# Kernel tuning notes

Hardware: AMD Instinct MI355X
Metric: run time of the kernel (lower is better)

## Reference

```python
import jax, jax.numpy as jnp
import numpy as np

FREQ = 10000.0

def _abs_pos(T, d, freq):
    # AP[t, 2i] = sin(t / freq**(2i/d)), AP[t, 2i+1] = cos(...), i in [0, T//2)
    pos = jnp.arange(T, dtype=jnp.float32)[:, None]          # [T,1]
    i = jnp.arange(T // 2, dtype=jnp.float32)[None, :]       # [1,T/2]
    angle = pos / (freq ** (2.0 * i / d))                    # [T,T/2]
    return jnp.stack([jnp.sin(angle), jnp.cos(angle)], axis=-1).reshape(T, T)

def setup_inputs() -> dict:
    key = jax.random.key(0)
    k0, k1, k2, k3, k4 = jax.random.split(key, 5)
    T, d, H, dh = 4096, 1024, 8, 128
    s = 1.0 / np.sqrt(d).astype(np.float32)
    return {
        "x": jax.random.normal(k0, (T, d), jnp.float32),
        "Wq": jax.random.normal(k1, (H, dh, d), jnp.float32) * s,
        "Wk": jax.random.normal(k2, (H, dh, d), jnp.float32) * s,
        "Wv": jax.random.normal(k3, (H, dh, d), jnp.float32) * s,
        "Wout": jax.random.normal(k4, (d, H * dh), jnp.float32) * s,
    }

def reference(x, Wq, Wk, Wv, Wout):
    # x: [T,d]; Wq/Wk/Wv: [H,dh,d] (torch Linear weight layout, bias=False); Wout: [d, H*dh]
    T, d = x.shape
    Q = jnp.einsum('td,hed->hte', x, Wq)                     # [H,T,dh]
    K = jnp.einsum('td,hed->hte', x, Wk)
    V = jnp.einsum('td,hed->hte', x, Wv)
    energies = jnp.einsum('hte,hse->hts', Q, K)              # [H,T,T] (no 1/sqrt(dh) scaling, as in source)
    energies = energies + _abs_pos(T, d, FREQ)[None]         # absolute sinusoidal bias added to scores
    att = jax.nn.softmax(energies, axis=-1)                  # [H,T,T]
    # dropout(p=0.5) is identity in eval mode; reference runs in eval mode
    y = jnp.einsum('hts,hse->hte', att, V)                   # [H,T,dh]
    y = jnp.transpose(y, (1, 0, 2)).reshape(T, -1)           # concat heads along feature dim -> [T, H*dh]
    y = y @ Wout.T                                           # [T,d]
    return y, att[-1]                                        # source returns last head's att_weights
```

## Files before the change

kernel.cpp:

```cpp
#include <hip/hip_runtime.h>
#include <math.h>

#define Tn 4096
#define Dm 1024
#define Hn 8
#define DH 128

typedef __bf16 bf16x8 __attribute__((ext_vector_type(8)));
typedef float f32x4 __attribute__((ext_vector_type(4)));

#define LOG2E 1.4426950408889634f
#define WEXP 0.025952563241307518f
#define WDECAY 0.31622776601683794f
#define PIO2 1.5707963267948966f

#define MFMA(a, b, c) __builtin_amdgcn_mfma_f32_16x16x32_bf16((a), (b), (c), 0, 0, 0)

#define GLOAD_LDS(g, l) __builtin_amdgcn_global_load_lds( \
    (__attribute__((address_space(1))) void*)(void*)(g),  \
    (__attribute__((address_space(3))) void*)(l), 16, 0, 0)

__global__ __launch_bounds__(256)
void split_kernel(const float* __restrict__ in, __bf16* __restrict__ hi,
                  __bf16* __restrict__ lo, int n4) {
    int idx = blockIdx.x * 256 + threadIdx.x;
    if (idx >= n4) return;
    float4 v = ((const float4*)in)[idx];
    __attribute__((aligned(8))) __bf16 h[4], l[4];
    h[0] = (__bf16)v.x; h[1] = (__bf16)v.y; h[2] = (__bf16)v.z; h[3] = (__bf16)v.w;
    l[0] = (__bf16)(v.x - (float)h[0]);
    l[1] = (__bf16)(v.y - (float)h[1]);
    l[2] = (__bf16)(v.z - (float)h[2]);
    l[3] = (__bf16)(v.w - (float)h[3]);
    *(float2*)&hi[(size_t)idx * 4] = *(float2*)h;
    *(float2*)&lo[(size_t)idx * 4] = *(float2*)l;
}

__global__ __launch_bounds__(256)
void vtrans_kernel(const __bf16* __restrict__ V, __bf16* __restrict__ Vt) {
    __shared__ __bf16 tile[64][80];
    int h = blockIdx.z, t0 = blockIdx.x * 64, e0 = blockIdx.y * 64;
    const __bf16* Vh = V + (size_t)h * Tn * DH;
    __bf16* Vth = Vt + (size_t)h * DH * Tn;
#pragma unroll
    for (int p = 0; p < 2; ++p) {
        int r = (threadIdx.x >> 3) + p * 32;
        int c = (threadIdx.x & 7) * 8;
        *(float4*)&tile[r][c] = *(const float4*)&Vh[(size_t)(t0 + r) * DH + e0 + c];
    }
    __syncthreads();
#pragma unroll
    for (int p = 0; p < 2; ++p) {
        int r = (threadIdx.x >> 3) + p * 32;
        int c = (threadIdx.x & 7) * 8;
        __attribute__((aligned(16))) __bf16 tmp[8];
#pragma unroll
        for (int j = 0; j < 8; ++j) tmp[j] = tile[c + j][r];
        *(float4*)&Vth[(size_t)(e0 + r) * Tn + t0 + c] = *(float4*)tmp;
    }
}

__device__ __forceinline__
void gemm_body(__bf16 (*smem)[128 * 32],
               const __bf16* __restrict__ Ahi, const __bf16* __restrict__ Alo,
               const __bf16* __restrict__ Bhi, const __bf16* __restrict__ Blo,
               int ldA, int ldB, int K, int m0, int n0, f32x4 acc[4][4]) {
    int tid = threadIdx.x;
    int lane = tid & 63, wid = tid >> 6;
    int wm = (wid >> 1) * 64, wn = (wid & 1) * 64;
    int lm = lane & 15, q = lane >> 4;
    int lr = lane >> 2;
    int lc = (lane & 3) * 8;
    const bool split = (Alo != nullptr);
    for (int k0 = 0; k0 < K; k0 += 32) {
        __syncthreads();
#pragma unroll
        for (int p = 0; p < 128; p += 64) {
            int rb = p + wid * 16;
            int r = rb + lr;
            GLOAD_LDS(&Ahi[(size_t)(m0 + r) * ldA + k0 + lc], &smem[0][rb * 32]);
            GLOAD_LDS(&Bhi[(size_t)(n0 + r) * ldB + k0 + lc], &smem[2][rb * 32]);
            if (split) {
                GLOAD_LDS(&Alo[(size_t)(m0 + r) * ldA + k0 + lc], &smem[1][rb * 32]);
                GLOAD_LDS(&Blo[(size_t)(n0 + r) * ldB + k0 + lc], &smem[3][rb * 32]);
            }
        }
        __syncthreads();
        bf16x8 ah[4], bh[4], al[4], bl[4];
#pragma unroll
        for (int mt = 0; mt < 4; ++mt) {
            ah[mt] = *(const bf16x8*)&smem[0][(wm + mt * 16 + lm) * 32 + q * 8];
            if (split)
                al[mt] = *(const bf16x8*)&smem[1][(wm + mt * 16 + lm) * 32 + q * 8];
        }
#pragma unroll
        for (int nt = 0; nt < 4; ++nt) {
            bh[nt] = *(const bf16x8*)&smem[2][(wn + nt * 16 + lm) * 32 + q * 8];
            if (split)
                bl[nt] = *(const bf16x8*)&smem[3][(wn + nt * 16 + lm) * 32 + q * 8];
        }
#pragma unroll
        for (int mt = 0; mt < 4; ++mt)
#pragma unroll
            for (int nt = 0; nt < 4; ++nt) {
                acc[mt][nt] = MFMA(ah[mt], bh[nt], acc[mt][nt]);
                if (split) {
                    acc[mt][nt] = MFMA(ah[mt], bl[nt], acc[mt][nt]);
                    acc[mt][nt] = MFMA(al[mt], bh[nt], acc[mt][nt]);
                }
            }
    }
}

__global__ __launch_bounds__(256)
void qkv_kernel(const __bf16* __restrict__ xhi, const __bf16* __restrict__ xlo,
                const __bf16* __restrict__ Wqh, const __bf16* __restrict__ Wql,
                const __bf16* __restrict__ Wkh, const __bf16* __restrict__ Wkl,
                const __bf16* __restrict__ Wvh, const __bf16* __restrict__ Wvl,
                __bf16* __restrict__ Qh, __bf16* __restrict__ Ql,
                __bf16* __restrict__ Kh, __bf16* __restrict__ Kl,
                __bf16* __restrict__ Vb) {
    __shared__ __align__(16) __bf16 smem[4][128 * 32];
    int z = blockIdx.z;
    const __bf16* Bh = (z == 0) ? Wqh : (z == 1) ? Wkh : Wvh;
    const __bf16* Bl = (z == 0) ? Wql : (z == 1) ? Wkl : Wvl;
    __bf16* Oh = (z == 0) ? Qh : (z == 1) ? Kh : Vb;
    __bf16* Ol = (z == 0) ? Ql : (z == 1) ? Kl : nullptr;
    int m0 = blockIdx.y * 128, n0 = blockIdx.x * 128;
    int tid = threadIdx.x, lane = tid & 63, wid = tid >> 6;
    int wm = (wid >> 1) * 64, wn = (wid & 1) * 64;
    int lm = lane & 15, q = lane >> 4;
    f32x4 acc[4][4];
#pragma unroll
    for (int i = 0; i < 4; ++i)
#pragma unroll
        for (int j = 0; j < 4; ++j) acc[i][j] = (f32x4){0.f, 0.f, 0.f, 0.f};
    gemm_body(smem, xhi, xlo, Bh, Bl, Dm, Dm, Dm, m0, n0, acc);
#pragma unroll
    for (int mt = 0; mt < 4; ++mt)
#pragma unroll
        for (int r = 0; r < 4; ++r) {
            int grow = m0 + wm + mt * 16 + q * 4 + r;
#pragma unroll
            for (int nt = 0; nt < 4; ++nt) {
                int gc = n0 + wn + nt * 16 + lm;
                int h = gc >> 7, e = gc & 127;
                size_t o = ((size_t)h * Tn + grow) * DH + e;
                float v = acc[mt][nt][r];
                __bf16 hv = (__bf16)v;
                Oh[o] = hv;
                if (Ol) Ol[o] = (__bf16)(v - (float)hv);
            }
        }
}

__global__ __launch_bounds__(256)
void gemm_out(const __bf16* __restrict__ Ahi, const __bf16* __restrict__ Alo,
              const __bf16* __restrict__ Bhi, const __bf16* __restrict__ Blo,
              float* __restrict__ C) {
    __shared__ __align__(16) __bf16 smem[4][128 * 32];
    int m0 = blockIdx.y * 128, n0 = blockIdx.x * 128;
    int tid = threadIdx.x, lane = tid & 63, wid = tid >> 6;
    int wm = (wid >> 1) * 64, wn = (wid & 1) * 64;
    int lm = lane & 15, q = lane >> 4;
    f32x4 acc[4][4];
#pragma unroll
    for (int i = 0; i < 4; ++i)
#pragma unroll
        for (int j = 0; j < 4; ++j) acc[i][j] = (f32x4){0.f, 0.f, 0.f, 0.f};
    gemm_body(smem, Ahi, Alo, Bhi, Blo, Dm, Dm, Dm, m0, n0, acc);
#pragma unroll
    for (int mt = 0; mt < 4; ++mt)
#pragma unroll
        for (int r = 0; r < 4; ++r) {
            int grow = m0 + wm + mt * 16 + q * 4 + r;
#pragma unroll
            for (int nt = 0; nt < 4; ++nt)
                C[(size_t)grow * Dm + n0 + wn + nt * 16 + lm] = acc[mt][nt][r];
        }
}

#define QK_STEP(SET, BUF, QIDX, NIT, NKC)                                     \
    {                                                                          \
        *(float4*)&Ks[BUF][0][sr][scc]      = SET##h0;                         \
        *(float4*)&Ks[BUF][1][sr][scc]      = SET##l0;                         \
        *(float4*)&Ks[BUF][0][sr + 64][scc] = SET##h1;                         \
        *(float4*)&Ks[BUF][1][sr + 64][scc] = SET##l1;                         \
        __syncthreads();                                                       \
        {                                                                      \
            size_t go0 = (size_t)((NIT) * 128 + sr) * DH + (NKC) * 32 + scc;   \
            size_t go1 = go0 + (size_t)64 * DH;                                \
            SET##h0 = *(const float4*)&Kh[go0];                                \
            SET##l0 = *(const float4*)&Kl[go0];                                \
            SET##h1 = *(const float4*)&Kh[go1];                                \
            SET##l1 = *(const float4*)&Kl[go1];                                \
        }                                                                      \
        __builtin_amdgcn_s_setprio(1);                                         \
        _Pragma("unroll")                                                      \
        for (int nt = 0; nt < 8; ++nt) {                                       \
            bf16x8 kbh = *(const bf16x8*)&Ks[BUF][0][nt * 16 + lm][q * 8];     \
            bf16x8 kbl = *(const bf16x8*)&Ks[BUF][1][nt * 16 + lm][q * 8];     \
            accS[nt] = MFMA(qfh[QIDX], kbh, accS[nt]);                         \
            accS[nt] = MFMA(qfh[QIDX], kbl, accS[nt]);                         \
            accS[nt] = MFMA(qfl[QIDX], kbh, accS[nt]);                         \
        }                                                                      \
        __builtin_amdgcn_s_setprio(0);                                         \
    }

__global__ __launch_bounds__(256, 2)
void flash_kernel(const __bf16* __restrict__ Qhi, const __bf16* __restrict__ Qlo,
                  const __bf16* __restrict__ Khi, const __bf16* __restrict__ Klo,
                  const __bf16* __restrict__ Vt, float* __restrict__ Opart,
                  float* __restrict__ mPart, float* __restrict__ lPart) {
    __shared__ __bf16 Ks[2][2][128][40];
    __shared__ __bf16 Ps[64][132];
    int bid = blockIdx.x;
    int h = bid & 7;
    int g = (bid >> 3) & 1;
    int m0 = (bid >> 4) * 64;
    int it0 = g * 16;
    const size_t TD = (size_t)Tn * DH;
    const __bf16* Qh = Qhi + h * TD;
    const __bf16* Ql = Qlo + h * TD;
    const __bf16* Kh = Khi + h * TD;
    const __bf16* Kl = Klo + h * TD;
    const __bf16* Vh = Vt + h * TD;
    float* Og = Opart + (size_t)g * Tn * Dm;

    int tid = threadIdx.x;
    int lane = tid & 63, wid = tid >> 6;
    int lm = lane & 15, q = lane >> 4;
    int wr0 = wid * 16;

    bf16x8 qfh[4], qfl[4];
#pragma unroll
    for (int kc = 0; kc < 4; ++kc) {
        size_t o = (size_t)(m0 + wr0 + lm) * DH + kc * 32 + q * 8;
        qfh[kc] = *(const bf16x8*)&Qh[o];
        qfl[kc] = *(const bf16x8*)&Ql[o];
    }

    f32x4 accO[8];
#pragma unroll
    for (int nt = 0; nt < 8; ++nt) accO[nt] = (f32x4){0.f, 0.f, 0.f, 0.f};
    float mrow[4], lrow[4];
#pragma unroll
    for (int r = 0; r < 4; ++r) { mrow[r] = -3.0e38f; lrow[r] = 0.f; }

    int sr = tid >> 2;
    int scc = (tid & 3) * 8;
    bool iscos = (lm & 1);
    float wv[8];
#pragma unroll
    for (int nt = 0; nt < 8; ++nt)
        wv[nt] = exp2f(-(float)(((g << 11) + nt * 16 + lm) >> 1) * WEXP);
    float tf[4];
#pragma unroll
    for (int r = 0; r < 4; ++r) tf[r] = (float)(m0 + wr0 + q * 4 + r);

    size_t voff[8];
#pragma unroll
    for (int nt = 0; nt < 8; ++nt)
        voff[nt] = (size_t)(nt * 16 + lm) * Tn + q * 8;

    float4 kah0, kal0, kah1, kal1, kbh0, kbl0, kbh1, kbl1;
    {
        size_t g0 = (size_t)(it0 * 128 + sr) * DH + scc;
        size_t g1 = g0 + (size_t)64 * DH;
        kah0 = *(const float4*)&Kh[g0]; kal0 = *(const float4*)&Kl[g0];
        kah1 = *(const float4*)&Kh[g1]; kal1 = *(const float4*)&Kl[g1];
        size_t h0_ = g0 + 32, h1_ = g1 + 32;
        kbh0 = *(const float4*)&Kh[h0_]; kbl0 = *(const float4*)&Kl[h0_];
        kbh1 = *(const float4*)&Kh[h1_]; kbl1 = *(const float4*)&Kl[h1_];
    }

    for (int it = it0; it < it0 + 16; ++it) {
        int s0 = it * 128;
        int itn = (it < it0 + 15) ? it + 1 : it;
        f32x4 accS[8];
#pragma unroll
        for (int nt = 0; nt < 8; ++nt) accS[nt] = (f32x4){0.f, 0.f, 0.f, 0.f};

        QK_STEP(ka, 0, 0, it, 2)
        QK_STEP(kb, 1, 1, it, 3)
        QK_STEP(ka, 0, 2, itn, 0)
        QK_STEP(kb, 1, 3, itn, 1)

        bf16x8 vrel[8];
#pragma unroll
        for (int nt = 0; nt < 8; ++nt)
            vrel[nt] = *(const bf16x8*)&Vh[voff[nt] + s0];

        float rmax[4];
#pragma unroll
        for (int r = 0; r < 4; ++r) {
            float mx = -3.0e38f;
#pragma unroll
            for (int nt = 0; nt < 8; ++nt) {
                float ang = tf[r] * wv[nt];
                float b = __sinf(iscos ? ang + PIO2 : ang);
                float v = accS[nt][r] + b;
                accS[nt][r] = v;
                mx = fmaxf(mx, v);
            }
            rmax[r] = mx;
        }
#pragma unroll
        for (int off = 1; off < 16; off <<= 1)
#pragma unroll
            for (int r = 0; r < 4; ++r)
                rmax[r] = fmaxf(rmax[r], __shfl_xor(rmax[r], off));
        float alpha[4], rsum[4];
#pragma unroll
        for (int r = 0; r < 4; ++r) {
            float mn = fmaxf(mrow[r], rmax[r]);
            alpha[r] = exp2f((mrow[r] - mn) * LOG2E);
            mrow[r] = mn;
            rsum[r] = 0.f;
        }
#pragma unroll
        for (int nt = 0; nt < 8; ++nt)
#pragma unroll
            for (int r = 0; r < 4; ++r) {
                float p = exp2f((accS[nt][r] - mrow[r]) * LOG2E);
                accS[nt][r] = p;
                rsum[r] += p;
            }
#pragma unroll
        for (int off = 1; off < 16; off <<= 1)
#pragma unroll
            for (int r = 0; r < 4; ++r)
                rsum[r] += __shfl_xor(rsum[r], off);
#pragma unroll
        for (int r = 0; r < 4; ++r)
            lrow[r] = lrow[r] * alpha[r] + rsum[r];
#pragma unroll
        for (int nt = 0; nt < 8; ++nt)
#pragma unroll
            for (int r = 0; r < 4; ++r)
                accO[nt][r] *= alpha[r];

#pragma unroll
        for (int nt = 0; nt < 8; ++nt)
#pragma unroll
            for (int r = 0; r < 4; ++r)
                Ps[wr0 + q * 4 + r][nt * 16 + lm] = (__bf16)accS[nt][r];

#pragma unroll
        for (int kc = 0; kc < 4; ++kc) {
            bf16x8 pa = *(const bf16x8*)&Ps[wr0 + lm][kc * 32 + q * 8];
            bf16x8 vcur[8];
#pragma unroll
            for (int nt = 0; nt < 8; ++nt) vcur[nt] = vrel[nt];
            if (kc < 3) {
#pragma unroll
                for (int nt = 0; nt < 8; ++nt)
                    vrel[nt] = *(const bf16x8*)&Vh[voff[nt] + s0 + (kc + 1) * 32];
            }
            __builtin_amdgcn_s_setprio(1);
#pragma unroll
            for (int nt = 0; nt < 8; ++nt)
                accO[nt] = MFMA(pa, vcur[nt], accO[nt]);
            __builtin_amdgcn_s_setprio(0);
        }

#pragma unroll
        for (int nt = 0; nt < 8; ++nt) wv[nt] *= WDECAY;
    }

#pragma unroll
    for (int r = 0; r < 4; ++r) {
        int t = m0 + wr0 + q * 4 + r;
#pragma unroll
        for (int nt = 0; nt < 8; ++nt)
            Og[(size_t)t * Dm + h * DH + nt * 16 + lm] = accO[nt][r];
        if (lm == 0) {
            mPart[(size_t)(g * Hn + h) * Tn + t] = mrow[r];
            lPart[(size_t)(g * Hn + h) * Tn + t] = lrow[r];
        }
    }
}

__global__ __launch_bounds__(256)
void combine_kernel(const float* __restrict__ Opart,
                    const float* __restrict__ mPart, const float* __restrict__ lPart,
                    __bf16* __restrict__ yhi, __bf16* __restrict__ ylo,
                    float* __restrict__ mM, float* __restrict__ lL) {
    int idx = blockIdx.x * 256 + threadIdx.x;
    int t = idx >> 8;
    int c4 = idx & 255;
    int c = c4 * 4;
    int h = c >> 7;
    float m0 = mPart[(size_t)h * Tn + t];
    float m1 = mPart[(size_t)(Hn + h) * Tn + t];
    float l0 = lPart[(size_t)h * Tn + t];
    float l1 = lPart[(size_t)(Hn + h) * Tn + t];
    float m = fmaxf(m0, m1);
    float w0 = exp2f((m0 - m) * LOG2E);
    float w1 = exp2f((m1 - m) * LOG2E);
    float l = l0 * w0 + l1 * w1;
    float inv = 1.0f / l;
    w0 *= inv; w1 *= inv;
    float4 a = ((const float4*)Opart)[idx];
    float4 b = ((const float4*)(Opart + (size_t)Tn * Dm))[idx];
    float y[4] = {a.x * w0 + b.x * w1, a.y * w0 + b.y * w1,
                  a.z * w0 + b.z * w1, a.w * w0 + b.w * w1};
    __attribute__((aligned(8))) __bf16 hh[4], ll[4];
#pragma unroll
    for (int j = 0; j < 4; ++j) {
        hh[j] = (__bf16)y[j];
        ll[j] = (__bf16)(y[j] - (float)hh[j]);
    }
    *(float2*)&yhi[(size_t)idx * 4] = *(float2*)hh;
    *(float2*)&ylo[(size_t)idx * 4] = *(float2*)ll;
    if (h == 7 && (c & 127) == 0) { mM[t] = m; lL[t] = l; }
}

__global__ __launch_bounds__(256)
void att_kernel(const __bf16* __restrict__ Ahi, const __bf16* __restrict__ Alo,
                const __bf16* __restrict__ Bhi, const __bf16* __restrict__ Blo,
                const float* __restrict__ mM, const float* __restrict__ lL,
                float* __restrict__ att) {
    __shared__ __align__(16) char shraw[34816];
    __bf16 (*smem)[128 * 32] = reinterpret_cast<__bf16(*)[128 * 32]>(shraw);
    float (*Ls)[68] = reinterpret_cast<float(*)[68]>(shraw);

    int m0 = blockIdx.y * 128, n0 = blockIdx.x * 128;
    int tid = threadIdx.x, lane = tid & 63, wid = tid >> 6;
    int wm = (wid >> 1) * 64, wn = (wid & 1) * 64;
    int lm = lane & 15, q = lane >> 4;
    f32x4 acc[4][4];
#pragma unroll
    for (int i = 0; i < 4; ++i)
#pragma unroll
        for (int j = 0; j < 4; ++j) acc[i][j] = (f32x4){0.f, 0.f, 0.f, 0.f};
    gemm_body(smem, Ahi, Alo, Bhi, Blo, DH, DH, DH, m0, n0, acc);

    float wv[4];
#pragma unroll
    for (int nt = 0; nt < 4; ++nt) {
        int s = n0 + wn + nt * 16 + lm;
        wv[nt] = exp2f(-(float)(s >> 1) * WEXP);
    }
    int par = lm & 1;
#pragma unroll
    for (int mt = 0; mt < 4; ++mt)
#pragma unroll
        for (int r = 0; r < 4; ++r) {
            int t = m0 + wm + mt * 16 + q * 4 + r;
            float tf = (float)t;
            float mr = mM[t];
            float linv = 1.0f / lL[t];
#pragma unroll
            for (int nt = 0; nt < 4; ++nt) {
                float ang = tf * wv[nt];
                float bias = __sinf(par ? ang + PIO2 : ang);
                acc[mt][nt][r] = exp2f((acc[mt][nt][r] + bias - mr) * LOG2E) * linv;
            }
        }

#pragma unroll
    for (int p = 0; p < 2; ++p) {
        __syncthreads();
        if ((wid & 1) == p) {
#pragma unroll
            for (int mt = 0; mt < 4; ++mt)
#pragma unroll
                for (int r = 0; r < 4; ++r)
#pragma unroll
                    for (int nt = 0; nt < 4; ++nt)
                        Ls[wm + mt * 16 + q * 4 + r][nt * 16 + lm] = acc[mt][nt][r];
        }
        __syncthreads();
#pragma unroll
        for (int j = 0; j < 8; ++j) {
            int row = j * 16 + (tid >> 4);
            int col = (tid & 15) * 4;
            float4 v = *(float4*)&Ls[row][col];
            *(float4*)&att[(size_t)(m0 + row) * Tn + n0 + p * 64 + col] = v;
        }
    }
}

extern "C" void kernel_launch(void* const* d_in, const int* in_sizes, int n_in,
                              void* d_out, int out_size, void* d_ws, size_t ws_size,
                              hipStream_t stream) {
    (void)in_sizes; (void)n_in; (void)out_size; (void)ws_size;
    const float* x    = (const float*)d_in[0];
    const float* Wq   = (const float*)d_in[1];
    const float* Wk   = (const float*)d_in[2];
    const float* Wv   = (const float*)d_in[3];
    const float* Wout = (const float*)d_in[4];

    float* out_y   = (float*)d_out;
    float* out_att = out_y + (size_t)Tn * Dm;

    const size_t MB = 1ull << 20;
    char* W = (char*)d_ws;
    __bf16* xhi  = (__bf16*)(W + 0 * MB);
    __bf16* xlo  = (__bf16*)(W + 8 * MB);
    __bf16* Wqhi = (__bf16*)(W + 16 * MB);
    __bf16* Wqlo = (__bf16*)(W + 18 * MB);
    __bf16* Wkhi = (__bf16*)(W + 20 * MB);
    __bf16* Wklo = (__bf16*)(W + 22 * MB);
    __bf16* Wvhi = (__bf16*)(W + 24 * MB);
    __bf16* Wvlo = (__bf16*)(W + 26 * MB);
    __bf16* Wohi = (__bf16*)(W + 28 * MB);
    __bf16* Wolo = (__bf16*)(W + 30 * MB);
    __bf16* Qhi  = (__bf16*)(W + 32 * MB);
    __bf16* Qlo  = (__bf16*)(W + 40 * MB);
    __bf16* Khi  = (__bf16*)(W + 48 * MB);
    __bf16* Klo  = (__bf16*)(W + 56 * MB);
    __bf16* Vb   = (__bf16*)(W + 64 * MB);
    __bf16* Vt   = (__bf16*)(W + 72 * MB);
    float*  mM    = (float*)(W + 80 * MB);
    float*  lL    = (float*)(W + 81 * MB);
    float*  mPart = (float*)(W + 82 * MB);
    float*  lPart = (float*)(W + 83 * MB);
    float*  Opart = (float*)(W + 84 * MB);
    __bf16* yhhi  = (__bf16*)(W + 116 * MB);
    __bf16* yhlo  = (__bf16*)(W + 124 * MB);

    dim3 blk(256);

    split_kernel<<<dim3(Tn * Dm / 4 / 256), blk, 0, stream>>>(x, xhi, xlo, Tn * Dm / 4);
    split_kernel<<<dim3(Dm * Dm / 4 / 256), blk, 0, stream>>>(Wq, Wqhi, Wqlo, Dm * Dm / 4);
    split_kernel<<<dim3(Dm * Dm / 4 / 256), blk, 0, stream>>>(Wk, Wkhi, Wklo, Dm * Dm / 4);
    split_kernel<<<dim3(Dm * Dm / 4 / 256), blk, 0, stream>>>(Wv, Wvhi, Wvlo, Dm * Dm / 4);
    split_kernel<<<dim3(Dm * Dm / 4 / 256), blk, 0, stream>>>(Wout, Wohi, Wolo, Dm * Dm / 4);

    qkv_kernel<<<dim3(Dm / 128, Tn / 128, 3), blk, 0, stream>>>(
        xhi, xlo, Wqhi, Wqlo, Wkhi, Wklo, Wvhi, Wvlo,
        Qhi, Qlo, Khi, Klo, Vb);
    vtrans_kernel<<<dim3(Tn / 64, DH / 64, Hn), blk, 0, stream>>>(Vb, Vt);

    flash_kernel<<<dim3(1024), blk, 0, stream>>>(Qhi, Qlo, Khi, Klo, Vt,
                                                 Opart, mPart, lPart);

    combine_kernel<<<dim3(Tn * Dm / 4 / 256), blk, 0, stream>>>(
        Opart, mPart, lPart, yhhi, yhlo, mM, lL);

    const size_t TD = (size_t)Tn * DH;
    att_kernel<<<dim3(Tn / 128, Tn / 128), blk, 0, stream>>>(
        Qhi + 7 * TD, Qlo + 7 * TD, Khi + 7 * TD, Klo + 7 * TD, mM, lL, out_att);

    gemm_out<<<dim3(Dm / 128, Tn / 128), blk, 0, stream>>>(yhhi, yhlo, Wohi, Wolo, out_y);
}
```

Baseline: 578.2 us.

## Drop flash split-KV and combine kernel; add lazy softmax rescaling

The flash kernel no longer splits the key range into two halves. Each block now walks all 32 key tiles and writes normalized bf16 hi/lo outputs plus the head-7 m/l stats directly, so the fp32 partial buffers and the separate combine kernel go away. It also adds a lazy-rescale rule: the running max and the accumulator rescale are updated only when a row max grows by more than a threshold, which skips exp and multiply work most iterations. The trade-off is a grid cut from 1024 to 512 blocks, which lowers parallelism on a large-CU GPU. The threshold also lets unnormalized exponentials grow up to e^8, while att_kernel relies on the stored m/l staying consistent.

```diff
diff --git a/kernel.cpp b/kernel.cpp
--- a/kernel.cpp
+++ b/kernel.cpp
@@ -210,22 +210,20 @@
 __global__ __launch_bounds__(256, 2)
 void flash_kernel(const __bf16* __restrict__ Qhi, const __bf16* __restrict__ Qlo,
                   const __bf16* __restrict__ Khi, const __bf16* __restrict__ Klo,
-                  const __bf16* __restrict__ Vt, float* __restrict__ Opart,
-                  float* __restrict__ mPart, float* __restrict__ lPart) {
+                  const __bf16* __restrict__ Vt,
+                  __bf16* __restrict__ yhi, __bf16* __restrict__ ylo,
+                  float* __restrict__ mM, float* __restrict__ lL) {
     __shared__ __bf16 Ks[2][2][128][40];
     __shared__ __bf16 Ps[64][132];
     int bid = blockIdx.x;
     int h = bid & 7;
-    int g = (bid >> 3) & 1;
-    int m0 = (bid >> 4) * 64;
-    int it0 = g * 16;
+    int m0 = (bid >> 3) * 64;
     const size_t TD = (size_t)Tn * DH;
     const __bf16* Qh = Qhi + h * TD;
     const __bf16* Ql = Qlo + h * TD;
     const __bf16* Kh = Khi + h * TD;
     const __bf16* Kl = Klo + h * TD;
     const __bf16* Vh = Vt + h * TD;
-    float* Og = Opart + (size_t)g * Tn * Dm;
 
     int tid = threadIdx.x;
     int lane = tid & 63, wid = tid >> 6;
@@ -253,7 +251,7 @@
     float wv[8];
 #pragma unroll
     for (int nt = 0; nt < 8; ++nt)
-        wv[nt] = exp2f(-(float)(((g << 11) + nt * 16 + lm) >> 1) * WEXP);
+        wv[nt] = exp2f(-(float)((nt * 16 + lm) >> 1) * WEXP);
     float tf[4];
 #pragma unroll
     for (int r = 0; r < 4; ++r) tf[r] = (float)(m0 + wr0 + q * 4 + r);
@@ -265,7 +263,7 @@
 
     float4 kah0, kal0, kah1, kal1, kbh0, kbl0, kbh1, kbl1;
     {
-        size_t g0 = (size_t)(it0 * 128 + sr) * DH + scc;
+        size_t g0 = (size_t)sr * DH + scc;
         size_t g1 = g0 + (size_t)64 * DH;
         kah0 = *(const float4*)&Kh[g0]; kal0 = *(const float4*)&Kl[g0];
         kah1 = *(const float4*)&Kh[g1]; kal1 = *(const float4*)&Kl[g1];
@@ -274,9 +272,9 @@
         kbh1 = *(const float4*)&Kh[h1_]; kbl1 = *(const float4*)&Kl[h1_];
     }
 
-    for (int it = it0; it < it0 + 16; ++it) {
+    for (int it = 0; it < 32; ++it) {
         int s0 = it * 128;
-        int itn = (it < it0 + 15) ? it + 1 : it;
+        int itn = (it < 31) ? it + 1 : it;
         f32x4 accS[8];
 #pragma unroll
         for (int nt = 0; nt < 8; ++nt) accS[nt] = (f32x4){0.f, 0.f, 0.f, 0.f};
@@ -310,14 +308,26 @@
 #pragma unroll
             for (int r = 0; r < 4; ++r)
                 rmax[r] = fmaxf(rmax[r], __shfl_xor(rmax[r], off));
-        float alpha[4], rsum[4];
-#pragma unroll
-        for (int r = 0; r < 4; ++r) {
-            float mn = fmaxf(mrow[r], rmax[r]);
-            alpha[r] = exp2f((mrow[r] - mn) * LOG2E);
-            mrow[r] = mn;
-            rsum[r] = 0.f;
-        }
+        bool need = (rmax[0] > mrow[0] + 8.0f) || (rmax[1] > mrow[1] + 8.0f) ||
+                    (rmax[2] > mrow[2] + 8.0f) || (rmax[3] > mrow[3] + 8.0f);
+        if (__any(need)) {
+            float alpha[4];
+#pragma unroll
+            for (int r = 0; r < 4; ++r) {
+                float mn = fmaxf(mrow[r], rmax[r]);
+                alpha[r] = exp2f((mrow[r] - mn) * LOG2E);
+                mrow[r] = mn;
+                lrow[r] *= alpha[r];
+            }
+#pragma unroll
+            for (int nt = 0; nt < 8; ++nt)
+#pragma unroll
+                for (int r = 0; r < 4; ++r)
+                    accO[nt][r] *= alpha[r];
+        }
+        float rsum[4];
+#pragma unroll
+        for (int r = 0; r < 4; ++r) rsum[r] = 0.f;
 #pragma unroll
         for (int nt = 0; nt < 8; ++nt)
 #pragma unroll
@@ -333,12 +343,7 @@
                 rsum[r] += __shfl_xor(rsum[r], off);
 #pragma unroll
         for (int r = 0; r < 4; ++r)
-            lrow[r] = lrow[r] * alpha[r] + rsum[r];
-#pragma unroll
-        for (int nt = 0; nt < 8; ++nt)
-#pragma unroll
-            for (int r = 0; r < 4; ++r)
-                accO[nt][r] *= alpha[r];
+            lrow[r] += rsum[r];
 
 #pragma unroll
         for (int nt = 0; nt < 8; ++nt)
@@ -370,50 +375,21 @@
 
 #pragma unroll
     for (int r = 0; r < 4; ++r) {
+        float inv = 1.0f / lrow[r];
         int t = m0 + wr0 + q * 4 + r;
 #pragma unroll
-        for (int nt = 0; nt < 8; ++nt)
-            Og[(size_t)t * Dm + h * DH + nt * 16 + lm] = accO[nt][r];
-        if (lm == 0) {
-            mPart[(size_t)(g * Hn + h) * Tn + t] = mrow[r];
-            lPart[(size_t)(g * Hn + h) * Tn + t] = lrow[r];
-        }
-    }
-}
-
-__global__ __launch_bounds__(256)
-void combine_kernel(const float* __restrict__ Opart,
-                    const float* __restrict__ mPart, const float* __restrict__ lPart,
-                    __bf16* __restrict__ yhi, __bf16* __restrict__ ylo,
-                    float* __restrict__ mM, float* __restrict__ lL) {
-    int idx = blockIdx.x * 256 + threadIdx.x;
-    int t = idx >> 8;
-    int c4 = idx & 255;
-    int c = c4 * 4;
-    int h = c >> 7;
-    float m0 = mPart[(size_t)h * Tn + t];
-    float m1 = mPart[(size_t)(Hn + h) * Tn + t];
-    float l0 = lPart[(size_t)h * Tn + t];
-    float l1 = lPart[(size_t)(Hn + h) * Tn + t];
-    float m = fmaxf(m0, m1);
-    float w0 = exp2f((m0 - m) * LOG2E);
-    float w1 = exp2f((m1 - m) * LOG2E);
-    float l = l0 * w0 + l1 * w1;
-    float inv = 1.0f / l;
-    w0 *= inv; w1 *= inv;
-    float4 a = ((const float4*)Opart)[idx];
-    float4 b = ((const float4*)(Opart + (size_t)Tn * Dm))[idx];
-    float y[4] = {a.x * w0 + b.x * w1, a.y * w0 + b.y * w1,
-                  a.z * w0 + b.z * w1, a.w * w0 + b.w * w1};
-    __attribute__((aligned(8))) __bf16 hh[4], ll[4];
-#pragma unroll
-    for (int j = 0; j < 4; ++j) {
-        hh[j] = (__bf16)y[j];
-        ll[j] = (__bf16)(y[j] - (float)hh[j]);
-    }
-    *(float2*)&yhi[(size_t)idx * 4] = *(float2*)hh;
-    *(float2*)&ylo[(size_t)idx * 4] = *(float2*)ll;
-    if (h == 7 && (c & 127) == 0) { mM[t] = m; lL[t] = l; }
+        for (int nt = 0; nt < 8; ++nt) {
+            float v = accO[nt][r] * inv;
+            __bf16 hv = (__bf16)v;
+            size_t o = (size_t)t * Dm + h * DH + nt * 16 + lm;
+            yhi[o] = hv;
+            ylo[o] = (__bf16)(v - (float)hv);
+        }
+        if (h == 7 && lm == 0) {
+            mM[t] = mrow[r];
+            lL[t] = lrow[r];
+        }
+    }
 }
 
 __global__ __launch_bounds__(256)
@@ -513,13 +489,10 @@
     __bf16* Klo  = (__bf16*)(W + 56 * MB);
     __bf16* Vb   = (__bf16*)(W + 64 * MB);
     __bf16* Vt   = (__bf16*)(W + 72 * MB);
-    float*  mM    = (float*)(W + 80 * MB);
-    float*  lL    = (float*)(W + 81 * MB);
-    float*  mPart = (float*)(W + 82 * MB);
-    float*  lPart = (float*)(W + 83 * MB);
-    float*  Opart = (float*)(W + 84 * MB);
-    __bf16* yhhi  = (__bf16*)(W + 116 * MB);
-    __bf16* yhlo  = (__bf16*)(W + 124 * MB);
+    float*  mM   = (float*)(W + 80 * MB);
+    float*  lL   = (float*)(W + 81 * MB);
+    __bf16* yhhi = (__bf16*)(W + 116 * MB);
+    __bf16* yhlo = (__bf16*)(W + 124 * MB);
 
     dim3 blk(256);
 
@@ -534,11 +507,8 @@
         Qhi, Qlo, Khi, Klo, Vb);
     vtrans_kernel<<<dim3(Tn / 64, DH / 64, Hn), blk, 0, stream>>>(Vb, Vt);
 
-    flash_kernel<<<dim3(1024), blk, 0, stream>>>(Qhi, Qlo, Khi, Klo, Vt,
-                                                 Opart, mPart, lPart);
-
-    combine_kernel<<<dim3(Tn * Dm / 4 / 256), blk, 0, stream>>>(
-        Opart, mPart, lPart, yhhi, yhlo, mM, lL);
+    flash_kernel<<<dim3(512), blk, 0, stream>>>(Qhi, Qlo, Khi, Klo, Vt,
+                                                yhhi, yhlo, mM, lL);
 
     const size_t TD = (size_t)Tn * DH;
     att_kernel<<<dim3(Tn / 128, Tn / 128), blk, 0, stream>>>(
```

Result: no change. 568.3 us (-1.7%).
